# Performance work log

Hardware: AMD Instinct MI355X
Metric: run time of the kernel (lower is better)

Reference implementation:

```python
import jax, jax.numpy as jnp
import numpy as np

B, D, C, S = 65536, 128, 10, 2
LAMBDA_E, LAMBDA_OD = 0.1, 0.036
GAMMA_E, GAMMA_OD = 2.0, 2.0
STEP_SIZE = 1000.0


def setup_inputs() -> dict:
    key = jax.random.key(0)
    ks = jax.random.split(key, 12)
    inp = {
        "mean_t": jax.random.normal(ks[0], (B, D), jnp.float32),
        "mean_s": jax.random.normal(ks[1], (B, D), jnp.float32),
        "log_std_t": jax.random.normal(ks[2], (B, D), jnp.float32),
        "log_std_s": jax.random.normal(ks[3], (B, D), jnp.float32),
        "y_zt": jax.random.normal(ks[4], (B, C), jnp.float32),
        "s_zt": jax.random.normal(ks[5], (B, S), jnp.float32),
        "eps_prior_t": jax.random.normal(ks[6], (B, D), jnp.float32),
        "eps_prior_s": jax.random.normal(ks[7], (B, D), jnp.float32),
        "eps_t": jax.random.normal(ks[8], (B, D), jnp.float32),
        "eps_s": jax.random.normal(ks[9], (B, D), jnp.float32),
        "target": jax.random.randint(ks[10], (B,), 0, C, jnp.int64),
        "current_step": 500,
    }
    return inp


def _kld_batchmean(log_p, t):
    # torch KLDivLoss(reduction='batchmean'): sum(t * (log t - log_p)) / batch
    return jnp.sum(t * (jnp.log(t) - log_p)) / t.shape[0]


def reference(mean_t, mean_s, log_std_t, log_std_s, y_zt, s_zt,
              eps_prior_t, eps_prior_s, eps_t, eps_s, target, current_step):
    # CIFAR10 branch: cross entropy on task logits
    logp_y = jax.nn.log_softmax(y_zt, axis=1)
    L_t = -jnp.mean(jnp.take_along_axis(logp_y, target[:, None], axis=1))

    # entropy loss on sensitive discriminator output
    sm = jax.nn.softmax(s_zt, axis=1)
    lsm = jax.nn.log_softmax(s_zt, axis=1)
    Loss_e = -jnp.sum(sm * lsm) / s_zt.shape[0]

    # prior samples: N(0, I) and N(1, I)  (mean_tensors(zeros, ones))
    prior_t = eps_prior_t            # mean 0
    prior_s = 1.0 + eps_prior_s      # mean 1

    # encoder samples: MVN(mean, diag(exp(log_std))) -> std = exp(0.5*log_std)
    # torch .sample() is non-differentiable -> stop_gradient
    enc_t = jax.lax.stop_gradient(mean_t + jnp.exp(0.5 * log_std_t) * eps_t)
    enc_s = jax.lax.stop_gradient(mean_s + jnp.exp(0.5 * log_std_s) * eps_s)

    L_zt = _kld_batchmean(jax.nn.log_softmax(prior_t, axis=1), jax.nn.softmax(enc_t, axis=1))
    L_zs = _kld_batchmean(jax.nn.log_softmax(prior_s, axis=1), jax.nn.softmax(enc_s, axis=1))

    frac = current_step / STEP_SIZE
    lam_e = LAMBDA_E * GAMMA_E ** frac
    lam_od = LAMBDA_OD * GAMMA_OD ** frac
    return L_t + lam_e * Loss_e + lam_od * (L_zt + L_zs)
```

## Files before the change

kernel.cpp:

```cpp
#include <hip/hip_runtime.h>
#include <hip/hip_bf16.h>
#include <math.h>

#define BATCH   65536
#define NCLS    10
#define NBLOCKS 2048
#define PAIRS_PER_WAVE 4


__global__ __launch_bounds__(256) void crit_main(
    const float* __restrict__ mean_t,      const float* __restrict__ mean_s,
    const float* __restrict__ log_std_t,   const float* __restrict__ log_std_s,
    const float* __restrict__ y_zt,        const float* __restrict__ s_zt,
    const float* __restrict__ eps_prior_t, const float* __restrict__ eps_prior_s,
    const float* __restrict__ eps_t,       const float* __restrict__ eps_s,
    const int*   __restrict__ target,
    double*      __restrict__ ws_partial)
{
    const int tid  = threadIdx.x;
    const int lane = tid & 63;
    const int sub  = lane & 31;
    const int half = lane >> 5;
    const int gwave = blockIdx.x * 4 + (tid >> 6);
    const int base  = gwave * PAIRS_PER_WAVE;

    const float4* MT = (const float4*)mean_t;
    const float4* LT = (const float4*)log_std_t;
    const float4* ET = (const float4*)eps_t;
    const float4* PT = (const float4*)eps_prior_t;
    const float4* MS = (const float4*)mean_s;
    const float4* LS = (const float4*)log_std_s;
    const float4* ES = (const float4*)eps_s;
    const float4* PS = (const float4*)eps_prior_s;

    double acc_ce = 0.0, acc_H = 0.0, acc_kl = 0.0;

    float4 cur[8];
    int tgt_cur = 0;
    {
        const int fidx = base * 64 + lane;
        cur[0] = MT[fidx]; cur[1] = LT[fidx]; cur[2] = ET[fidx]; cur[3] = PT[fidx];
        cur[4] = MS[fidx]; cur[5] = LS[fidx]; cur[6] = ES[fidx]; cur[7] = PS[fidx];
        if (sub == 0) tgt_cur = target[base * 2 + half];
    }

    #pragma unroll
    for (int i = 0; i < PAIRS_PER_WAVE; ++i) {
        const int pair = base + i;

        float4 nxt[8];
        int tgt_nxt = 0;
        if (i + 1 < PAIRS_PER_WAVE) {
            const int fidx = (pair + 1) * 64 + lane;
            nxt[0] = MT[fidx]; nxt[1] = LT[fidx]; nxt[2] = ET[fidx]; nxt[3] = PT[fidx];
            nxt[4] = MS[fidx]; nxt[5] = LS[fidx]; nxt[6] = ES[fidx]; nxt[7] = PS[fidx];
            if (sub == 0) tgt_nxt = target[(pair + 1) * 2 + half];
        }

        const int r = pair * 2 + half;
        float2 y01, y23, y45, y67, y89, s2;
        float  yt = 0.0f;
        if (sub == 0) {
            const float* yr = y_zt + (size_t)r * NCLS;
            y01 = *(const float2*)(yr + 0);
            y23 = *(const float2*)(yr + 2);
            y45 = *(const float2*)(yr + 4);
            y67 = *(const float2*)(yr + 6);
            y89 = *(const float2*)(yr + 8);
            s2  = *(const float2*)(s_zt + (size_t)r * 2);
            yt  = yr[tgt_cur];
        }

        const float4 mu_t = cur[0], ls_t = cur[1], ep_t = cur[2], pr_t = cur[3];
        const float4 mu_s = cur[4], ls_s = cur[5], ep_s = cur[6], pr_s = cur[7];

        float et0 = fmaf(__expf(0.5f * ls_t.x), ep_t.x, mu_t.x);
        float et1 = fmaf(__expf(0.5f * ls_t.y), ep_t.y, mu_t.y);
        float et2 = fmaf(__expf(0.5f * ls_t.z), ep_t.z, mu_t.z);
        float et3 = fmaf(__expf(0.5f * ls_t.w), ep_t.w, mu_t.w);
        float es0 = fmaf(__expf(0.5f * ls_s.x), ep_s.x, mu_s.x);
        float es1 = fmaf(__expf(0.5f * ls_s.y), ep_s.y, mu_s.y);
        float es2 = fmaf(__expf(0.5f * ls_s.z), ep_s.z, mu_s.z);
        float es3 = fmaf(__expf(0.5f * ls_s.w), ep_s.w, mu_s.w);

        float xt0 = __expf(et0), xt1 = __expf(et1), xt2 = __expf(et2), xt3 = __expf(et3);
        float xs0 = __expf(es0), xs1 = __expf(es1), xs2 = __expf(es2), xs3 = __expf(es3);

        float red[6];
        red[0] = (xt0 + xt1) + (xt2 + xt3);
        red[1] = (__expf(pr_t.x) + __expf(pr_t.y)) + (__expf(pr_t.z) + __expf(pr_t.w));
        red[2] = (xt0 * (et0 - pr_t.x) + xt1 * (et1 - pr_t.y))
               + (xt2 * (et2 - pr_t.z) + xt3 * (et3 - pr_t.w));
        red[3] = (xs0 + xs1) + (xs2 + xs3);
        red[4] = (__expf(pr_s.x) + __expf(pr_s.y)) + (__expf(pr_s.z) + __expf(pr_s.w));
        red[5] = (xs0 * (es0 - pr_s.x) + xs1 * (es1 - pr_s.y))
               + (xs2 * (es2 - pr_s.z) + xs3 * (es3 - pr_s.w));

        #pragma unroll
        for (int m = 16; m >= 1; m >>= 1) {
            #pragma unroll
            for (int j = 0; j < 6; ++j) red[j] += __shfl_xor(red[j], m, 64);
        }

        const float rt = 1.0f / red[0];
        const float rs = 1.0f / red[3];
        const float kl = red[2] * rt + __logf(red[1] * rt)
                       + red[5] * rs + __logf(red[4] * rs);

        if (sub == 0) {
            float Z = (__expf(y01.x) + __expf(y01.y)) + (__expf(y23.x) + __expf(y23.y))
                    + (__expf(y45.x) + __expf(y45.y)) + (__expf(y67.x) + __expf(y67.y))
                    + (__expf(y89.x) + __expf(y89.y));
            float ce = __logf(Z) - yt;

            float za = __expf(s2.x), zb = __expf(s2.y);
            float Zs = za + zb;
            float lses = __logf(Zs);
            float H  = -((za / Zs) * (s2.x - lses) + (zb / Zs) * (s2.y - lses));

            acc_ce += (double)ce;
            acc_H  += (double)H;
            acc_kl += (double)kl;
        }

        if (i + 1 < PAIRS_PER_WAVE) {
            #pragma unroll
            for (int j = 0; j < 8; ++j) cur[j] = nxt[j];
            tgt_cur = tgt_nxt;
        }
    }

    __shared__ double sh[8][3];
    if (sub == 0) {
        const int slot = tid >> 5;
        sh[slot][0] = acc_ce;
        sh[slot][1] = acc_H;
        sh[slot][2] = acc_kl;
    }
    __syncthreads();
    if (tid == 0) {
        double c = 0.0, h = 0.0, k = 0.0;
        #pragma unroll
        for (int i = 0; i < 8; ++i) { c += sh[i][0]; h += sh[i][1]; k += sh[i][2]; }
        ws_partial[blockIdx.x * 3 + 0] = c;
        ws_partial[blockIdx.x * 3 + 1] = h;
        ws_partial[blockIdx.x * 3 + 2] = k;
    }
}

__global__ __launch_bounds__(256) void crit_reduce(
    const double* __restrict__ ws_partial,
    const int*    __restrict__ step_ptr,
    float*        __restrict__ out,
    int nblocks)
{
    const int tid = threadIdx.x;
    double c = 0.0, h = 0.0, k = 0.0;
    for (int i = tid; i < nblocks; i += 256) {
        c += ws_partial[3 * i + 0];
        h += ws_partial[3 * i + 1];
        k += ws_partial[3 * i + 2];
    }
    __shared__ double sc[256], sh_[256], sk[256];
    sc[tid] = c; sh_[tid] = h; sk[tid] = k;
    __syncthreads();
    for (int s = 128; s > 0; s >>= 1) {
        if (tid < s) { sc[tid] += sc[tid + s]; sh_[tid] += sh_[tid + s]; sk[tid] += sk[tid + s]; }
        __syncthreads();
    }
    if (tid == 0) {
        double frac  = (double)step_ptr[0] / 1000.0;
        double lam_e  = 0.1   * exp2(frac);
        double lam_od = 0.036 * exp2(frac);
        out[0] = (float)((sc[0] + lam_e * sh_[0] + lam_od * sk[0]) / (double)BATCH);
    }
}

extern "C" void kernel_launch(void* const* d_in, const int* in_sizes, int n_in,
                              void* d_out, int out_size, void* d_ws, size_t ws_size,
                              hipStream_t stream) {
    const float* mean_t      = (const float*)d_in[0];
    const float* mean_s      = (const float*)d_in[1];
    const float* log_std_t   = (const float*)d_in[2];
    const float* log_std_s   = (const float*)d_in[3];
    const float* y_zt        = (const float*)d_in[4];
    const float* s_zt        = (const float*)d_in[5];
    const float* eps_prior_t = (const float*)d_in[6];
    const float* eps_prior_s = (const float*)d_in[7];
    const float* eps_t       = (const float*)d_in[8];
    const float* eps_s       = (const float*)d_in[9];
    const int*   target      = (const int*)d_in[10];
    const int*   step_ptr    = (const int*)d_in[11];

    double* ws_partial = (double*)d_ws;
    float*  out        = (float*)d_out;

    crit_main<<<NBLOCKS, 256, 0, stream>>>(
        mean_t, mean_s, log_std_t, log_std_s, y_zt, s_zt,
        eps_prior_t, eps_prior_s, eps_t, eps_s, target, ws_partial);
    crit_reduce<<<1, 256, 0, stream>>>(ws_partial, step_ptr, out, NBLOCKS);
}
```

Measured before the change: 268.9 us.

## Issue all row loads up front and batch shuffle reductions across pairs

```diff
diff --git a/kernel.cpp b/kernel.cpp
--- a/kernel.cpp
+++ b/kernel.cpp
@@ -5,10 +5,12 @@
 #define BATCH   65536
 #define NCLS    10
 #define NBLOCKS 2048
-#define PAIRS_PER_WAVE 4
-
-
-__global__ __launch_bounds__(256) void crit_main(
+#define PAIRS   4
+
+typedef float vf4 __attribute__((ext_vector_type(4)));
+
+
+__global__ __launch_bounds__(256, 4) void crit_main(
     const float* __restrict__ mean_t,      const float* __restrict__ mean_s,
     const float* __restrict__ log_std_t,   const float* __restrict__ log_std_s,
     const float* __restrict__ y_zt,        const float* __restrict__ s_zt,
@@ -22,120 +24,124 @@
     const int sub  = lane & 31;
     const int half = lane >> 5;
     const int gwave = blockIdx.x * 4 + (tid >> 6);
-    const int base  = gwave * PAIRS_PER_WAVE;
-
-    const float4* MT = (const float4*)mean_t;
-    const float4* LT = (const float4*)log_std_t;
-    const float4* ET = (const float4*)eps_t;
-    const float4* PT = (const float4*)eps_prior_t;
-    const float4* MS = (const float4*)mean_s;
-    const float4* LS = (const float4*)log_std_s;
-    const float4* ES = (const float4*)eps_s;
-    const float4* PS = (const float4*)eps_prior_s;
-
-    double acc_ce = 0.0, acc_H = 0.0, acc_kl = 0.0;
-
-    float4 cur[8];
-    int tgt_cur = 0;
-    {
-        const int fidx = base * 64 + lane;
-        cur[0] = MT[fidx]; cur[1] = LT[fidx]; cur[2] = ET[fidx]; cur[3] = PT[fidx];
-        cur[4] = MS[fidx]; cur[5] = LS[fidx]; cur[6] = ES[fidx]; cur[7] = PS[fidx];
-        if (sub == 0) tgt_cur = target[base * 2 + half];
-    }
-
+    const int base  = gwave * PAIRS;
+
+    const vf4* MT = (const vf4*)mean_t;
+    const vf4* LT = (const vf4*)log_std_t;
+    const vf4* ET = (const vf4*)eps_t;
+    const vf4* PT = (const vf4*)eps_prior_t;
+    const vf4* MS = (const vf4*)mean_s;
+    const vf4* LS = (const vf4*)log_std_s;
+    const vf4* ES = (const vf4*)eps_s;
+    const vf4* PS = (const vf4*)eps_prior_s;
+
+    int    tgt[PAIRS];
+    float2 y0[PAIRS], y1[PAIRS], y2[PAIRS], y3[PAIRS], y4[PAIRS], s2[PAIRS];
+    if (sub == 0) {
+        #pragma unroll
+        for (int i = 0; i < PAIRS; ++i) {
+            const int r = (base + i) * 2 + half;
+            tgt[i] = target[r];
+            const float* yr = y_zt + (size_t)r * NCLS;
+            y0[i] = *(const float2*)(yr + 0);
+            y1[i] = *(const float2*)(yr + 2);
+            y2[i] = *(const float2*)(yr + 4);
+            y3[i] = *(const float2*)(yr + 6);
+            y4[i] = *(const float2*)(yr + 8);
+            s2[i] = *(const float2*)(s_zt + (size_t)r * 2);
+        }
+    }
+
+    float part[PAIRS][6];
     #pragma unroll
-    for (int i = 0; i < PAIRS_PER_WAVE; ++i) {
-        const int pair = base + i;
-
-        float4 nxt[8];
-        int tgt_nxt = 0;
-        if (i + 1 < PAIRS_PER_WAVE) {
-            const int fidx = (pair + 1) * 64 + lane;
-            nxt[0] = MT[fidx]; nxt[1] = LT[fidx]; nxt[2] = ET[fidx]; nxt[3] = PT[fidx];
-            nxt[4] = MS[fidx]; nxt[5] = LS[fidx]; nxt[6] = ES[fidx]; nxt[7] = PS[fidx];
-            if (sub == 0) tgt_nxt = target[(pair + 1) * 2 + half];
+    for (int i = 0; i < PAIRS; ++i) {
+        const int fidx = (base + i) * 64 + lane;
+
+        const vf4 mu_t = __builtin_nontemporal_load(&MT[fidx]);
+        const vf4 ls_t = __builtin_nontemporal_load(&LT[fidx]);
+        const vf4 ep_t = __builtin_nontemporal_load(&ET[fidx]);
+        const vf4 pr_t = __builtin_nontemporal_load(&PT[fidx]);
+        const vf4 mu_s = __builtin_nontemporal_load(&MS[fidx]);
+        const vf4 ls_s = __builtin_nontemporal_load(&LS[fidx]);
+        const vf4 ep_s = __builtin_nontemporal_load(&ES[fidx]);
+        const vf4 pr_s = __builtin_nontemporal_load(&PS[fidx]);
+
+        const float et0 = fmaf(__expf(0.5f * ls_t.x), ep_t.x, mu_t.x);
+        const float et1 = fmaf(__expf(0.5f * ls_t.y), ep_t.y, mu_t.y);
+        const float et2 = fmaf(__expf(0.5f * ls_t.z), ep_t.z, mu_t.z);
+        const float et3 = fmaf(__expf(0.5f * ls_t.w), ep_t.w, mu_t.w);
+        const float es0 = fmaf(__expf(0.5f * ls_s.x), ep_s.x, mu_s.x);
+        const float es1 = fmaf(__expf(0.5f * ls_s.y), ep_s.y, mu_s.y);
+        const float es2 = fmaf(__expf(0.5f * ls_s.z), ep_s.z, mu_s.z);
+        const float es3 = fmaf(__expf(0.5f * ls_s.w), ep_s.w, mu_s.w);
+
+        const float xt0 = __expf(et0), xt1 = __expf(et1);
+        const float xt2 = __expf(et2), xt3 = __expf(et3);
+        const float xs0 = __expf(es0), xs1 = __expf(es1);
+        const float xs2 = __expf(es2), xs3 = __expf(es3);
+
+        part[i][0] = (xt0 + xt1) + (xt2 + xt3);
+        part[i][1] = (__expf(pr_t.x) + __expf(pr_t.y)) + (__expf(pr_t.z) + __expf(pr_t.w));
+        part[i][2] = (xt0 * (et0 - pr_t.x) + xt1 * (et1 - pr_t.y))
+                   + (xt2 * (et2 - pr_t.z) + xt3 * (et3 - pr_t.w));
+        part[i][3] = (xs0 + xs1) + (xs2 + xs3);
+        part[i][4] = (__expf(pr_s.x) + __expf(pr_s.y)) + (__expf(pr_s.z) + __expf(pr_s.w));
+        part[i][5] = (xs0 * (es0 - pr_s.x) + xs1 * (es1 - pr_s.y))
+                   + (xs2 * (es2 - pr_s.z) + xs3 * (es3 - pr_s.w));
+    }
+
+    #pragma unroll
+    for (int m = 16; m >= 1; m >>= 1) {
+        #pragma unroll
+        for (int i = 0; i < PAIRS; ++i) {
+            #pragma unroll
+            for (int j = 0; j < 6; ++j) part[i][j] += __shfl_xor(part[i][j], m, 64);
         }
-
-        const int r = pair * 2 + half;
-        float2 y01, y23, y45, y67, y89, s2;
-        float  yt = 0.0f;
-        if (sub == 0) {
-            const float* yr = y_zt + (size_t)r * NCLS;
-            y01 = *(const float2*)(yr + 0);
-            y23 = *(const float2*)(yr + 2);
-            y45 = *(const float2*)(yr + 4);
-            y67 = *(const float2*)(yr + 6);
-            y89 = *(const float2*)(yr + 8);
-            s2  = *(const float2*)(s_zt + (size_t)r * 2);
-            yt  = yr[tgt_cur];
-        }
-
-        const float4 mu_t = cur[0], ls_t = cur[1], ep_t = cur[2], pr_t = cur[3];
-        const float4 mu_s = cur[4], ls_s = cur[5], ep_s = cur[6], pr_s = cur[7];
-
-        float et0 = fmaf(__expf(0.5f * ls_t.x), ep_t.x, mu_t.x);
-        float et1 = fmaf(__expf(0.5f * ls_t.y), ep_t.y, mu_t.y);
-        float et2 = fmaf(__expf(0.5f * ls_t.z), ep_t.z, mu_t.z);
-        float et3 = fmaf(__expf(0.5f * ls_t.w), ep_t.w, mu_t.w);
-        float es0 = fmaf(__expf(0.5f * ls_s.x), ep_s.x, mu_s.x);
-        float es1 = fmaf(__expf(0.5f * ls_s.y), ep_s.y, mu_s.y);
-        float es2 = fmaf(__expf(0.5f * ls_s.z), ep_s.z, mu_s.z);
-        float es3 = fmaf(__expf(0.5f * ls_s.w), ep_s.w, mu_s.w);
-
-        float xt0 = __expf(et0), xt1 = __expf(et1), xt2 = __expf(et2), xt3 = __expf(et3);
-        float xs0 = __expf(es0), xs1 = __expf(es1), xs2 = __expf(es2), xs3 = __expf(es3);
-
-        float red[6];
-        red[0] = (xt0 + xt1) + (xt2 + xt3);
-        red[1] = (__expf(pr_t.x) + __expf(pr_t.y)) + (__expf(pr_t.z) + __expf(pr_t.w));
-        red[2] = (xt0 * (et0 - pr_t.x) + xt1 * (et1 - pr_t.y))
-               + (xt2 * (et2 - pr_t.z) + xt3 * (et3 - pr_t.w));
-        red[3] = (xs0 + xs1) + (xs2 + xs3);
-        red[4] = (__expf(pr_s.x) + __expf(pr_s.y)) + (__expf(pr_s.z) + __expf(pr_s.w));
-        red[5] = (xs0 * (es0 - pr_s.x) + xs1 * (es1 - pr_s.y))
-               + (xs2 * (es2 - pr_s.z) + xs3 * (es3 - pr_s.w));
-
-        #pragma unroll
-        for (int m = 16; m >= 1; m >>= 1) {
-            #pragma unroll
-            for (int j = 0; j < 6; ++j) red[j] += __shfl_xor(red[j], m, 64);
-        }
-
-        const float rt = 1.0f / red[0];
-        const float rs = 1.0f / red[3];
-        const float kl = red[2] * rt + __logf(red[1] * rt)
-                       + red[5] * rs + __logf(red[4] * rs);
-
-        if (sub == 0) {
-            float Z = (__expf(y01.x) + __expf(y01.y)) + (__expf(y23.x) + __expf(y23.y))
-                    + (__expf(y45.x) + __expf(y45.y)) + (__expf(y67.x) + __expf(y67.y))
-                    + (__expf(y89.x) + __expf(y89.y));
-            float ce = __logf(Z) - yt;
-
-            float za = __expf(s2.x), zb = __expf(s2.y);
-            float Zs = za + zb;
-            float lses = __logf(Zs);
-            float H  = -((za / Zs) * (s2.x - lses) + (zb / Zs) * (s2.y - lses));
-
-            acc_ce += (double)ce;
-            acc_H  += (double)H;
-            acc_kl += (double)kl;
-        }
-
-        if (i + 1 < PAIRS_PER_WAVE) {
-            #pragma unroll
-            for (int j = 0; j < 8; ++j) cur[j] = nxt[j];
-            tgt_cur = tgt_nxt;
+    }
+
+    float kl_sum = 0.0f, ce_sum = 0.0f, H_sum = 0.0f;
+    #pragma unroll
+    for (int i = 0; i < PAIRS; ++i) {
+        const float rt = 1.0f / part[i][0];
+        const float rs = 1.0f / part[i][3];
+        kl_sum += part[i][2] * rt + __logf(part[i][1] * rt)
+                + part[i][5] * rs + __logf(part[i][4] * rs);
+    }
+    if (sub == 0) {
+        #pragma unroll
+        for (int i = 0; i < PAIRS; ++i) {
+            const int t = tgt[i];
+            float yt = y0[i].x;
+            yt = (t == 1) ? y0[i].y : yt;
+            yt = (t == 2) ? y1[i].x : yt;
+            yt = (t == 3) ? y1[i].y : yt;
+            yt = (t == 4) ? y2[i].x : yt;
+            yt = (t == 5) ? y2[i].y : yt;
+            yt = (t == 6) ? y3[i].x : yt;
+            yt = (t == 7) ? y3[i].y : yt;
+            yt = (t == 8) ? y4[i].x : yt;
+            yt = (t == 9) ? y4[i].y : yt;
+
+            const float Z = (__expf(y0[i].x) + __expf(y0[i].y))
+                          + (__expf(y1[i].x) + __expf(y1[i].y))
+                          + (__expf(y2[i].x) + __expf(y2[i].y))
+                          + (__expf(y3[i].x) + __expf(y3[i].y))
+                          + (__expf(y4[i].x) + __expf(y4[i].y));
+            ce_sum += __logf(Z) - yt;
+
+            const float za = __expf(s2[i].x), zb = __expf(s2[i].y);
+            const float Zs = za + zb;
+            const float lses = __logf(Zs);
+            H_sum += -((za / Zs) * (s2[i].x - lses) + (zb / Zs) * (s2[i].y - lses));
         }
     }
 
     __shared__ double sh[8][3];
     if (sub == 0) {
         const int slot = tid >> 5;
-        sh[slot][0] = acc_ce;
-        sh[slot][1] = acc_H;
-        sh[slot][2] = acc_kl;
+        sh[slot][0] = (double)ce_sum;
+        sh[slot][1] = (double)H_sum;
+        sh[slot][2] = (double)kl_sum;
     }
     __syncthreads();
     if (tid == 0) {
```

Result: faster. 243.2 us (-9.5%).
